# Optimization experiments

Hardware: AMD Instinct MI355X
Metric: run time of the kernel (lower is better)

## Reference

```python
import jax, jax.numpy as jnp
import numpy as np
from jax import lax

D = 2048; H = 32; N = 64; S = 2048
LW = 64; LA = 64; LG = 128; LV = 32


def _ln(z, w, b, eps):
    m = jnp.mean(z, axis=-1, keepdims=True)
    v = jnp.var(z, axis=-1, keepdims=True)
    return (z - m) * lax.rsqrt(v + eps) * w + b


def setup_inputs():
    ks = iter(jax.random.split(jax.random.key(0), 40))
    nrm = lambda shape, s=1.0: jax.random.normal(next(ks), shape, dtype=jnp.float32) * s
    return {
        "x": nrm((1, S, D)),
        "state1": nrm((D,)),
        "state2": nrm((H, N, N), 0.1),
        "v_first": nrm((S, H, N)),
        "ln1_w": jnp.ones((D,), jnp.float32),
        "ln1_b": jnp.zeros((D,), jnp.float32),
        "x_r": nrm((D,), 0.1), "x_w": nrm((D,), 0.1), "x_k": nrm((D,), 0.1),
        "x_v": nrm((D,), 0.1), "x_a": nrm((D,), 0.1), "x_g": nrm((D,), 0.1),
        "Wr": nrm((D, D), 0.02), "Wk": nrm((D, D), 0.02),
        "Wv": nrm((D, D), 0.02), "Wo": nrm((D, D), 0.02),
        "w1": nrm((D, LW), 0.02), "w2": nrm((LW, D), 0.05), "w0": nrm((D,), 0.1),
        "a1": nrm((D, LA), 0.02), "a2": nrm((LA, D), 0.05), "a0": nrm((D,), 0.1),
        "g1": nrm((D, LG), 0.02), "g2": nrm((LG, D), 0.05),
        "v1": nrm((D, LV), 0.02), "v2": nrm((LV, D), 0.05), "v0": nrm((D,), 0.1),
        "k_k": nrm((H, N), 0.5), "k_a": nrm((H, N), 0.5), "r_k": nrm((H, N), 0.5),
        "ln_x_w": jnp.ones((D,), jnp.float32),
        "ln_x_b": jnp.zeros((D,), jnp.float32),
    }


def _forward(x, state1, state2, v_first, ln1_w, ln1_b, x_r, x_w, x_k, x_v, x_a, x_g,
             Wr, Wk, Wv, Wo, w1, w2, w0, a1, a2, a0, g1, g2, v1, v2, v0,
             k_k, k_a, r_k, ln_x_w, ln_x_b):
    last_x = x
    xn = _ln(x, ln1_w, ln1_b, 1e-5)                      # (1,S,D)
    state1_out = xn[:, -1:]
    past = jnp.concatenate([state1.reshape(1, 1, D), xn[:, :-1]], axis=1)
    sx = past - xn                                        # token-shift delta
    xr = xn + sx * x_r; xw = xn + sx * x_w; xk = xn + sx * x_k
    xv = xn + sx * x_v; xa = xn + sx * x_a; xg = xn + sx * x_g
    r = (xr @ Wr.T).reshape(S, H, N)
    k = (xk @ Wk.T).reshape(S, H, N)
    v = (xv @ Wv.T).reshape(S, H, N)
    gate = jax.nn.sigmoid(xg @ g1) @ g2                   # (1,S,D)
    a = jax.nn.sigmoid((xa @ a1) @ a2 + a0).reshape(S, H, N)
    td = jnp.tanh(xw @ w1) @ w2 + w0
    w_dec = jnp.exp(-0.606531 * jax.nn.sigmoid(td)).reshape(S, H, N)
    kk = k * k_k
    kk = kk / jnp.maximum(jnp.linalg.norm(kk, axis=-1, keepdims=True), 1e-12)
    k = k * (1.0 + (a - 1.0) * k_a)
    # layer_id != 0: residual value mixing with v_first
    v = v + (v_first - v) * jax.nn.sigmoid(((xv @ v1) @ v2 + v0).reshape(S, H, N))
    b = kk * a
    a_neg = -kk

    def step(s, inp):
        # s: (H,N,N) state; each input (H,N)
        r_t, w_t, k_t, v_t, a_t, b_t = inp
        sa = jnp.einsum('hij,hj->hi', s, a_t)
        s = s * w_t[:, None, :] + sa[:, :, None] * b_t[:, None, :] + v_t[:, :, None] * k_t[:, None, :]
        return s, jnp.einsum('hij,hj->hi', s, r_t)

    state2_out, y = lax.scan(step, state2, (r, w_dec, k, v, a_neg, b))  # y: (S,H,N)
    o = _ln(y, 1.0, 0.0, 0.00064).reshape(1, S, D)       # ln_x (default affine)
    o = o * ln_x_w + ln_x_b
    rkv = (jnp.sum(r * k * r_k, axis=-1, keepdims=True) * v).reshape(1, S, D)
    o = (o + rkv) * gate
    o = o @ Wo.T
    return last_x + o, state1_out, state2_out


def reference(x, state1, state2, v_first, ln1_w, ln1_b, x_r, x_w, x_k, x_v, x_a, x_g,
              Wr, Wk, Wv, Wo, w1, w2, w0, a1, a2, a0, g1, g2, v1, v2, v0,
              k_k, k_a, r_k, ln_x_w, ln_x_b):
    return _forward(x, state1, state2, v_first, ln1_w, ln1_b, x_r, x_w, x_k, x_v, x_a, x_g,
                    Wr, Wk, Wv, Wo, w1, w2, w0, a1, a2, a0, g1, g2, v1, v2, v0,
                    k_k, k_a, r_k, ln_x_w, ln_x_b)
```

## Files before the change

### kernel.cpp

```cpp
#include <hip/hip_runtime.h>
#include <math.h>

#define kD 2048
#define kH 32
#define kN 64
#define kS 2048

typedef unsigned short ushort_t;
typedef unsigned int uint32;

__device__ __forceinline__ ushort_t f2bf(float f) {
  uint32 u = __float_as_uint(f);
  u += 0x7fffu + ((u >> 16) & 1u);
  return (ushort_t)(u >> 16);
}
__device__ __forceinline__ float bf2f(ushort_t u) {
  return __uint_as_float(((uint32)u) << 16);
}
__device__ __forceinline__ float sigm(float x) { return 1.f / (1.f + __expf(-x)); }

__global__ __launch_bounds__(256) void ln1_kernel(
    const float* __restrict__ x, const float* __restrict__ w, const float* __restrict__ b,
    ushort_t* __restrict__ xnbf, ushort_t* __restrict__ xprevbf,
    const float* __restrict__ state1, float* __restrict__ state1_out)
{
  int t = blockIdx.x;
  const float* row = x + (size_t)t * kD;
  float s = 0.f, s2 = 0.f;
  for (int d = threadIdx.x; d < kD; d += 256) {
    float v = row[d]; s += v; s2 += v * v;
  }
  #pragma unroll
  for (int o = 32; o > 0; o >>= 1) { s += __shfl_down(s, o); s2 += __shfl_down(s2, o); }
  __shared__ float ls[4], ls2[4];
  int wid = threadIdx.x >> 6;
  if ((threadIdx.x & 63) == 0) { ls[wid] = s; ls2[wid] = s2; }
  __syncthreads();
  s = ls[0] + ls[1] + ls[2] + ls[3];
  s2 = ls2[0] + ls2[1] + ls2[2] + ls2[3];
  float mean = s * (1.f / kD);
  float var = s2 * (1.f / kD) - mean * mean;
  float rstd = rsqrtf(var + 1e-5f);
  for (int d = threadIdx.x; d < kD; d += 256) {
    float v = (row[d] - mean) * rstd * w[d] + b[d];
    ushort_t bf = f2bf(v);
    xnbf[(size_t)t * kD + d] = bf;
    if (t < kS - 1) xprevbf[(size_t)(t + 1) * kD + d] = bf;
    else state1_out[d] = v;
    if (t == 0) xprevbf[d] = f2bf(state1[d]);
  }
}

__global__ __launch_bounds__(256) void mix3_cvt(
    const ushort_t* __restrict__ xnbf, const ushort_t* __restrict__ xprevbf,
    const float* __restrict__ cr, const float* __restrict__ ck, const float* __restrict__ cv,
    ushort_t* __restrict__ Ar, ushort_t* __restrict__ Ak, ushort_t* __restrict__ Av)
{
  int t = blockIdx.x;
  size_t base = (size_t)t * kD;
  for (int d = threadIdx.x; d < kD; d += 256) {
    float c = bf2f(xnbf[base + d]);
    float dx = bf2f(xprevbf[base + d]) - c;
    Ar[base + d] = f2bf(c + dx * cr[d]);
    Ak[base + d] = f2bf(c + dx * ck[d]);
    Av[base + d] = f2bf(c + dx * cv[d]);
  }
}

struct CvtArgs { const float* src[3]; ushort_t* dst[3]; };
__global__ __launch_bounds__(256) void cvt_bf16_b(CvtArgs args)
{
  const float* in = args.src[blockIdx.y];
  ushort_t* out = args.dst[blockIdx.y];
  int idx = blockIdx.x * 256 + threadIdx.x;
  float4 v = ((const float4*)in)[idx];
  ushort_t o[4] = { f2bf(v.x), f2bf(v.y), f2bf(v.z), f2bf(v.w) };
  ((uint2*)out)[idx] = *(const uint2*)o;
}

typedef __bf16 bf16x8 __attribute__((ext_vector_type(8)));
typedef float f32x4 __attribute__((ext_vector_type(4)));

struct GemmArgs {
  const ushort_t* A[3];
  const ushort_t* B[3];
  float* C[3];
  const float* resid[3];
};

__global__ __launch_bounds__(256) void gemm_bf16_b(GemmArgs args)
{
  int z = blockIdx.z;
  const ushort_t* __restrict__ A = args.A[z];
  const ushort_t* __restrict__ B = args.B[z];
  float* __restrict__ C = args.C[z];
  const float* __restrict__ resid = args.resid[z];

  __shared__ __align__(16) ushort_t As[128 * 64];
  __shared__ __align__(16) ushort_t Bs[128 * 64];
  int tid = threadIdx.x;
  int w = tid >> 6, lane = tid & 63;
  int row0 = blockIdx.y * 128, col0 = blockIdx.x * 128;
  int wrow = (w >> 1) * 64, wcol = (w & 1) * 64;
  int quad = lane >> 4, r16 = lane & 15;
  f32x4 acc[4][4] = {};

  int lrow = lane >> 3;
  int lsw  = (lane & 7) ^ lrow;

  for (int k0 = 0; k0 < kD; k0 += 64) {
    #pragma unroll
    for (int n = 0; n < 4; n++) {
      int rr = w * 32 + n * 8 + lrow;
      int cc = k0 + lsw * 8;
      const ushort_t* ga = A + (size_t)(row0 + rr) * kD + cc;
      const ushort_t* gb = B + (size_t)(col0 + rr) * kD + cc;
      __builtin_amdgcn_global_load_lds(
          (const __attribute__((address_space(1))) uint32*)ga,
          (__attribute__((address_space(3))) uint32*)&As[(w * 32 + n * 8) * 64], 16, 0, 0);
      __builtin_amdgcn_global_load_lds(
          (const __attribute__((address_space(1))) uint32*)gb,
          (__attribute__((address_space(3))) uint32*)&Bs[(w * 32 + n * 8) * 64], 16, 0, 0);
    }
    __syncthreads();
    #pragma unroll
    for (int kk = 0; kk < 64; kk += 32) {
      bf16x8 af[4], bfr[4];
      #pragma unroll
      for (int i = 0; i < 4; i++) {
        int row = wrow + i * 16 + r16;
        int chunk = ((kk >> 3) + quad) ^ (r16 & 7);
        af[i] = *(const bf16x8*)&As[row * 64 + chunk * 8];
      }
      #pragma unroll
      for (int j = 0; j < 4; j++) {
        int row = wcol + j * 16 + r16;
        int chunk = ((kk >> 3) + quad) ^ (r16 & 7);
        bfr[j] = *(const bf16x8*)&Bs[row * 64 + chunk * 8];
      }
      #pragma unroll
      for (int i = 0; i < 4; i++)
        #pragma unroll
        for (int j = 0; j < 4; j++)
          acc[i][j] = __builtin_amdgcn_mfma_f32_16x16x32_bf16(af[i], bfr[j], acc[i][j], 0, 0, 0);
    }
    __syncthreads();
  }
  #pragma unroll
  for (int i = 0; i < 4; i++) {
    #pragma unroll
    for (int j = 0; j < 4; j++) {
      int col = col0 + wcol + j * 16 + r16;
      #pragma unroll
      for (int reg = 0; reg < 4; reg++) {
        int row = row0 + wrow + i * 16 + quad * 4 + reg;
        float v = acc[i][j][reg];
        if (resid) v += resid[(size_t)row * kD + col];
        C[(size_t)row * kD + col] = v;
      }
    }
  }
}

struct PrepW1Args { const float* w1[4]; const float* c[4]; ushort_t* B1; };
__global__ __launch_bounds__(256) void prep_w1(PrepW1Args a)
{
  __shared__ float tile[64][17];
  int k0 = blockIdx.x * 64;
  int col0 = blockIdx.y * 16;
  int z, lc0, L;
  if (col0 < 128)      { z = 0; lc0 = col0;       L = 128; }
  else if (col0 < 192) { z = 1; lc0 = col0 - 128; L = 64; }
  else if (col0 < 256) { z = 2; lc0 = col0 - 192; L = 64; }
  else if (col0 < 288) { z = 3; lc0 = col0 - 256; L = 32; }
  else z = -1;
  int tid = threadIdx.x;
  if (z >= 0) {
    const float* W = a.w1[z];
    const float* C = a.c[z];
    int cc = tid & 15, kk = tid >> 4;
    #pragma unroll
    for (int i = 0; i < 4; i++) {
      int k = k0 + kk + i * 16;
      int ksrc = k & (kD - 1);
      float cv = C[ksrc];
      float sc = (k < kD) ? (1.f - cv) : cv;
      tile[kk + i * 16][cc] = W[(size_t)ksrc * L + lc0 + cc] * sc;
    }
  }
  __syncthreads();
  int kk2 = tid & 63, cc2 = tid >> 6;
  #pragma unroll
  for (int i = 0; i < 4; i++) {
    int col = col0 + cc2 * 4 + i;
    float v = (z >= 0) ? tile[kk2][cc2 * 4 + i] : 0.f;
    a.B1[(size_t)col * 4096 + k0 + kk2] = f2bf(v);
  }
}

struct PrepW2Args { const float* w2[4]; ushort_t* B2[4]; int L[4]; };
__global__ __launch_bounds__(256) void prep_w2(PrepW2Args a)
{
  __shared__ float tile[64][17];
  int z = blockIdx.z;
  int L = a.L[z];
  int l0 = blockIdx.y * 16;
  if (l0 >= L) return;
  int j0 = blockIdx.x * 64;
  int tid = threadIdx.x;
  const float* W = a.w2[z];
  ushort_t* out = a.B2[z];
  int jj = tid & 63;
  #pragma unroll
  for (int i = 0; i < 4; i++) {
    int ll = (tid >> 6) * 4 + i;
    tile[jj][ll] = W[(size_t)(l0 + ll) * kD + j0 + jj];
  }
  __syncthreads();
  int ll2 = tid & 15;
  #pragma unroll
  for (int i = 0; i < 4; i++) {
    int jj2 = (tid >> 4) + i * 16;
    out[(size_t)(j0 + jj2) * L + l0 + ll2] = f2bf(tile[jj2][ll2]);
  }
}

__global__ __launch_bounds__(256) void gemm1_kernel(
    const ushort_t* __restrict__ xnbf, const ushort_t* __restrict__ xprevbf,
    const ushort_t* __restrict__ B1, ushort_t* __restrict__ H)
{
  __shared__ __align__(16) ushort_t As[128 * 64];
  __shared__ __align__(16) ushort_t Bs[64 * 64];
  int tid = threadIdx.x;
  int w = tid >> 6, lane = tid & 63;
  int col0 = blockIdx.x * 64, row0 = blockIdx.y * 128;
  int quad = lane >> 4, r16 = lane & 15;
  f32x4 acc[2][4] = {};
  int lrow = lane >> 3;
  int lsw = (lane & 7) ^ lrow;

  for (int k0 = 0; k0 < 4096; k0 += 64) {
    const ushort_t* Abase = (k0 < kD) ? (xnbf + k0) : (xprevbf + (k0 - kD));
    #pragma unroll
    for (int n = 0; n < 4; n++) {
      int rr = w * 32 + n * 8 + lrow;
      const ushort_t* ga = Abase + (size_t)(row0 + rr) * kD + lsw * 8;
      __builtin_amdgcn_global_load_lds(
          (const __attribute__((address_space(1))) uint32*)ga,
          (__attribute__((address_space(3))) uint32*)&As[(w * 32 + n * 8) * 64], 16, 0, 0);
    }
    #pragma unroll
    for (int n = 0; n < 2; n++) {
      int rr = w * 16 + n * 8 + lrow;
      const ushort_t* gb = B1 + (size_t)(col0 + rr) * 4096 + k0 + lsw * 8;
      __builtin_amdgcn_global_load_lds(
          (const __attribute__((address_space(1))) uint32*)gb,
          (__attribute__((address_space(3))) uint32*)&Bs[(w * 16 + n * 8) * 64], 16, 0, 0);
    }
    __syncthreads();
    #pragma unroll
    for (int kk = 0; kk < 64; kk += 32) {
      bf16x8 af[2], bfr[4];
      #pragma unroll
      for (int i = 0; i < 2; i++) {
        int row = w * 32 + i * 16 + r16;
        int chunk = ((kk >> 3) + quad) ^ (r16 & 7);
        af[i] = *(const bf16x8*)&As[row * 64 + chunk * 8];
      }
      #pragma unroll
      for (int j = 0; j < 4; j++) {
        int row = j * 16 + r16;
        int chunk = ((kk >> 3) + quad) ^ (r16 & 7);
        bfr[j] = *(const bf16x8*)&Bs[row * 64 + chunk * 8];
      }
      #pragma unroll
      for (int i = 0; i < 2; i++)
        #pragma unroll
        for (int j = 0; j < 4; j++)
          acc[i][j] = __builtin_amdgcn_mfma_f32_16x16x32_bf16(af[i], bfr[j], acc[i][j], 0, 0, 0);
    }
    __syncthreads();
  }
  #pragma unroll
  for (int i = 0; i < 2; i++) {
    #pragma unroll
    for (int j = 0; j < 4; j++) {
      int col = col0 + j * 16 + r16;
      #pragma unroll
      for (int reg = 0; reg < 4; reg++) {
        int row = row0 + w * 32 + i * 16 + quad * 4 + reg;
        float v = acc[i][j][reg];
        if (col < 128) v = sigm(v);
        else if (col >= 192 && col < 256) v = tanhf(v);
        H[(size_t)row * 320 + col] = f2bf(v);
      }
    }
  }
}

struct Gemm2Args {
  const ushort_t* H;
  const ushort_t* B2[4];
  int Aofs[4];
  int L[4];
  const float* bias[4];
  float* out[4];
  const float* vfirst;
};
__global__ __launch_bounds__(256) void gemm2_kernel(Gemm2Args a)
{
  int z = blockIdx.z;
  int L = a.L[z];
  int nch = L >> 3;
  int rs = __builtin_ctz(nch);
  int mask = (nch >= 8) ? 7 : (nch - 1);
  __shared__ __align__(16) ushort_t As[128 * 128];
  __shared__ __align__(16) ushort_t Bs[128 * 128];
  int tid = threadIdx.x;
  int w = tid >> 6, lane = tid & 63;
  int row0 = blockIdx.y * 128, col0 = blockIdx.x * 128;
  int wrow = (w >> 1) * 64, wcol = (w & 1) * 64;
  int quad = lane >> 4, r16 = lane & 15;
  const ushort_t* A = a.H + a.Aofs[z];
  const ushort_t* B = a.B2[z];

  int nld = (128 * nch) >> 8;
  for (int i = 0; i < nld; i++) {
    int c = i * 256 + w * 64 + lane;
    int row = c >> rs;
    int ch = c & (nch - 1);
    int gch = ch ^ (row & mask);
    __builtin_amdgcn_global_load_lds(
        (const __attribute__((address_space(1))) uint32*)(A + (size_t)(row0 + row) * 320 + gch * 8),
        (__attribute__((address_space(3))) uint32*)&As[(i * 256 + w * 64) * 8], 16, 0, 0);
    __builtin_amdgcn_global_load_lds(
        (const __attribute__((address_space(1))) uint32*)(B + (size_t)(col0 + row) * L + gch * 8),
        (__attribute__((address_space(3))) uint32*)&Bs[(i * 256 + w * 64) * 8], 16, 0, 0);
  }
  __syncthreads();

  f32x4 acc[4][4] = {};
  int ksteps = L >> 5;
  for (int ks = 0; ks < ksteps; ks++) {
    bf16x8 af[4], bfr[4];
    #pragma unroll
    for (int i = 0; i < 4; i++) {
      int row = wrow + i * 16 + r16;
      int slot = ((ks << 2) + quad) ^ (r16 & mask);
      af[i] = *(const bf16x8*)&As[row * L + slot * 8];
    }
    #pragma unroll
    for (int j = 0; j < 4; j++) {
      int row = wcol + j * 16 + r16;
      int slot = ((ks << 2) + quad) ^ (r16 & mask);
      bfr[j] = *(const bf16x8*)&Bs[row * L + slot * 8];
    }
    #pragma unroll
    for (int i = 0; i < 4; i++)
      #pragma unroll
      for (int j = 0; j < 4; j++)
        acc[i][j] = __builtin_amdgcn_mfma_f32_16x16x32_bf16(af[i], bfr[j], acc[i][j], 0, 0, 0);
  }

  const float* bias = a.bias[z];
  float* C = a.out[z];
  #pragma unroll
  for (int i = 0; i < 4; i++) {
    #pragma unroll
    for (int j = 0; j < 4; j++) {
      int col = col0 + wcol + j * 16 + r16;
      #pragma unroll
      for (int reg = 0; reg < 4; reg++) {
        int row = row0 + wrow + i * 16 + quad * 4 + reg;
        float s = acc[i][j][reg];
        size_t idx = (size_t)row * kD + col;
        if (z == 0) {
          C[idx] = s;
        } else if (z == 1) {
          C[idx] = sigm(s + bias[col]);
        } else if (z == 2) {
          C[idx] = __expf(-0.606531f * sigm(s + bias[col]));
        } else {
          float vv = C[idx];
          C[idx] = vv + (a.vfirst[idx] - vv) * sigm(s + bias[col]);
        }
      }
    }
  }
}

__global__ __launch_bounds__(256) void post_kernel(
    float* __restrict__ kArr, float* __restrict__ kkArr, float* __restrict__ bArr,
    const float* __restrict__ aArr, const float* __restrict__ k_k, const float* __restrict__ k_a)
{
  int gid = blockIdx.x * 4 + (threadIdx.x >> 6);
  int lane = threadIdx.x & 63;
  int h = gid & (kH - 1);
  size_t off = (size_t)gid * kN + lane;
  float kv = kArr[off];
  float kkv = kv * k_k[h * kN + lane];
  float ss = kkv * kkv;
  #pragma unroll
  for (int o = 32; o > 0; o >>= 1) ss += __shfl_xor(ss, o);
  float scale = 1.f / fmaxf(sqrtf(ss), 1e-12f);
  float kkf = kkv * scale;
  kkArr[off] = kkf;
  float av = aArr[off];
  bArr[off] = kkf * av;
  kArr[off] = kv * (1.f + (av - 1.f) * k_a[h * kN + lane]);
}

#define SLOT_F 336
#define NSLOT 24

__device__ __forceinline__ float row_allsum(float x) {
  int t;
  t = __builtin_amdgcn_update_dpp(0, __float_as_int(x), 0x121, 0xF, 0xF, true);
  x += __int_as_float(t);
  t = __builtin_amdgcn_update_dpp(0, __float_as_int(x), 0x122, 0xF, 0xF, true);
  x += __int_as_float(t);
  t = __builtin_amdgcn_update_dpp(0, __float_as_int(x), 0x124, 0xF, 0xF, true);
  x += __int_as_float(t);
  t = __builtin_amdgcn_update_dpp(0, __float_as_int(x), 0x128, 0xF, 0xF, true);
  x += __int_as_float(t);
  return x;
}

__global__ __launch_bounds__(320) void scan_kernel(
    const float* __restrict__ s0_in, const float* __restrict__ rA, const float* __restrict__ wA,
    const float* __restrict__ kA, const float* __restrict__ vA, const float* __restrict__ kkA,
    const float* __restrict__ bA, float* __restrict__ y, float* __restrict__ s_out)
{
  __shared__ __align__(16) float ring[NSLOT * SLOT_F];
  int blk = blockIdx.x;
  int h = blk >> 2;
  int i0 = (blk & 3) << 4;
  int wid = threadIdx.x >> 6;
  int lane = threadIdx.x & 63;
  int hv = h * kN;

  if (wid == 0) {
    const float* src0 = rA + hv;
    const float* src1 = wA + hv;
    const float* src2 = kA + hv;
    const float* src3 = kkA + hv;
    const float* src4 = bA + hv;
    const float* vsrc = vA + hv + i0;
    int slot = 0;
    #define ISSUE(t)                                                                     \
      {                                                                                  \
        float* sb = &ring[slot * SLOT_F];                                                \
        size_t go = (size_t)(t) * kD + lane;                                             \
        __builtin_amdgcn_global_load_lds(                                                \
            (const __attribute__((address_space(1))) uint32*)(src0 + go),                \
            (__attribute__((address_space(3))) uint32*)(sb + 0), 4, 0, 0);               \
        __builtin_amdgcn_global_load_lds(                                                \
            (const __attribute__((address_space(1))) uint32*)(src1 + go),                \
            (__attribute__((address_space(3))) uint32*)(sb + 64), 4, 0, 0);              \
        __builtin_amdgcn_global_load_lds(                                                \
            (const __attribute__((address_space(1))) uint32*)(src2 + go),                \
            (__attribute__((address_space(3))) uint32*)(sb + 128), 4, 0, 0);             \
        __builtin_amdgcn_global_load_lds(                                                \
            (const __attribute__((address_space(1))) uint32*)(src3 + go),                \
            (__attribute__((address_space(3))) uint32*)(sb + 192), 4, 0, 0);             \
        __builtin_amdgcn_global_load_lds(                                                \
            (const __attribute__((address_space(1))) uint32*)(src4 + go),                \
            (__attribute__((address_space(3))) uint32*)(sb + 256), 4, 0, 0);             \
        if (lane < 16)                                                                   \
          __builtin_amdgcn_global_load_lds(                                              \
              (const __attribute__((address_space(1))) uint32*)(vsrc + (size_t)(t) * kD + lane), \
              (__attribute__((address_space(3))) uint32*)(sb + 320), 4, 0, 0);           \
        slot++; if (slot == NSLOT) slot = 0;                                             \
      }
    for (int t = 0; t < 16; t++) ISSUE(t);
    __syncthreads();
    for (int ph = 0; ph < kS / 8; ph++) {
      int t0 = ph * 8 + 16;
      if (t0 < kS) {
        for (int s = 0; s < 8; s++) ISSUE(t0 + s);
      }
      __syncthreads();
    }
    #undef ISSUE
  } else {
    int col16 = lane & 15;
    int row = lane >> 4;
    int vidx = (wid - 1) * 4 + row;
    int i = i0 + vidx;
    int co = col16 * 4;
    size_t srow = ((size_t)(hv + i)) * kN + co;
    float4 sS = *(const float4*)(s0_in + srow);
    float* py = y + (size_t)(hv + i);

    __syncthreads();

    float4 Ar4, Aw4, Ak4, Akk4, Ab4; float Av1;
    float4 Br4, Bw4, Bk4, Bkk4, Bb4; float Bv1;

    #define LOADSLOT(sl, R, W, K, KK, B, V)                      \
      {                                                          \
        const float* sb = &ring[(sl) * SLOT_F];                  \
        R  = *(const float4*)(sb + co);                          \
        W  = *(const float4*)(sb + 64 + co);                     \
        K  = *(const float4*)(sb + 128 + co);                    \
        KK = *(const float4*)(sb + 192 + co);                    \
        B  = *(const float4*)(sb + 256 + co);                    \
        V  = sb[320 + vidx];                                     \
      }
    #define STEP(R, W, K, KK, B, V)                                       \
      {                                                                   \
        float sa = sS.x * KK.x + sS.y * KK.y + sS.z * KK.z + sS.w * KK.w; \
        sa = row_allsum(sa);                                              \
        sa = -sa;                                                         \
        sS.x = fmaf(sS.x, W.x, fmaf(sa, B.x, V * K.x));                   \
        sS.y = fmaf(sS.y, W.y, fmaf(sa, B.y, V * K.y));                   \
        sS.z = fmaf(sS.z, W.z, fmaf(sa, B.z, V * K.z));                   \
        sS.w = fmaf(sS.w, W.w, fmaf(sa, B.w, V * K.w));                   \
        float yv = sS.x * R.x + sS.y * R.y + sS.z * R.z + sS.w * R.w;     \
        yv = row_allsum(yv);                                              \
        if (col16 == 0) *py = yv;                                         \
        py += kD;                                                         \
      }

    LOADSLOT(0, Ar4, Aw4, Ak4, Akk4, Ab4, Av1);
    int slot = 1;
    for (int ph = 0; ph < kS / 8; ph++) {
      #pragma unroll
      for (int s = 0; s < 8; s += 2) {
        LOADSLOT(slot, Br4, Bw4, Bk4, Bkk4, Bb4, Bv1);
        slot++; if (slot == NSLOT) slot = 0;
        STEP(Ar4, Aw4, Ak4, Akk4, Ab4, Av1);
        LOADSLOT(slot, Ar4, Aw4, Ak4, Akk4, Ab4, Av1);
        slot++; if (slot == NSLOT) slot = 0;
        STEP(Br4, Bw4, Bk4, Bkk4, Bb4, Bv1);
      }
      __syncthreads();
    }
    #undef LOADSLOT
    #undef STEP
    *(float4*)(s_out + srow) = sS;
  }
}

__global__ __launch_bounds__(256) void out_kernel(
    const float* __restrict__ y, const float* __restrict__ rA, const float* __restrict__ kA,
    const float* __restrict__ vA, const float* __restrict__ r_k,
    const float* __restrict__ lnw, const float* __restrict__ lnb,
    const float* __restrict__ gate, ushort_t* __restrict__ Ay)
{
  int gid = blockIdx.x * 4 + (threadIdx.x >> 6);
  int lane = threadIdx.x & 63;
  int h = gid & (kH - 1);
  size_t off = (size_t)gid * kN + lane;
  float yv = y[off];
  float s = yv, s2 = yv * yv;
  #pragma unroll
  for (int o = 32; o > 0; o >>= 1) { s += __shfl_xor(s, o); s2 += __shfl_xor(s2, o); }
  float mean = s * (1.f / kN);
  float var = s2 * (1.f / kN) - mean * mean;
  float o1 = (yv - mean) * rsqrtf(var + 0.00064f);
  int d = h * kN + lane;
  float ov = o1 * lnw[d] + lnb[d];
  float p = rA[off] * kA[off] * r_k[d];
  #pragma unroll
  for (int o = 32; o > 0; o >>= 1) p += __shfl_xor(p, o);
  float rkv = p * vA[off];
  Ay[off] = f2bf((ov + rkv) * gate[off]);
}

extern "C" void kernel_launch(void* const* d_in, const int* in_sizes, int n_in,
                              void* d_out, int out_size, void* d_ws, size_t ws_size,
                              hipStream_t stream)
{
  const float* x      = (const float*)d_in[0];
  const float* state1 = (const float*)d_in[1];
  const float* state2 = (const float*)d_in[2];
  const float* vfirst = (const float*)d_in[3];
  const float* ln1w   = (const float*)d_in[4];
  const float* ln1b   = (const float*)d_in[5];
  const float* xr_c   = (const float*)d_in[6];
  const float* xw_c   = (const float*)d_in[7];
  const float* xk_c   = (const float*)d_in[8];
  const float* xv_c   = (const float*)d_in[9];
  const float* xa_c   = (const float*)d_in[10];
  const float* xg_c   = (const float*)d_in[11];
  const float* Wr     = (const float*)d_in[12];
  const float* Wk     = (const float*)d_in[13];
  const float* Wv     = (const float*)d_in[14];
  const float* Wo     = (const float*)d_in[15];
  const float* w1     = (const float*)d_in[16];
  const float* w2     = (const float*)d_in[17];
  const float* w0     = (const float*)d_in[18];
  const float* a1     = (const float*)d_in[19];
  const float* a2     = (const float*)d_in[20];
  const float* a0     = (const float*)d_in[21];
  const float* g1     = (const float*)d_in[22];
  const float* g2     = (const float*)d_in[23];
  const float* v1     = (const float*)d_in[24];
  const float* v2     = (const float*)d_in[25];
  const float* v0     = (const float*)d_in[26];
  const float* k_k    = (const float*)d_in[27];
  const float* k_a    = (const float*)d_in[28];
  const float* r_k    = (const float*)d_in[29];
  const float* lnxw   = (const float*)d_in[30];
  const float* lnxb   = (const float*)d_in[31];

  float* out0  = (float*)d_out;
  float* s1out = out0 + (size_t)kS * kD;
  float* s2out = s1out + kD;

  size_t SD = (size_t)kS * kD;
  float* ws  = (float*)d_ws;
  float* xnB = ws;
  float* rB  = ws + SD;
  float* kB  = ws + 2 * SD;
  float* vB  = ws + 3 * SD;
  float* wB  = ws + 4 * SD;
  float* aB  = ws + 5 * SD;
  float* kkB = ws + 6 * SD;
  float* bB  = ws + 7 * SD;
  float* gB  = ws + 8 * SD;
  float* yB  = ws + 9 * SD;

  ushort_t* xnbf    = (ushort_t*)xnB;
  ushort_t* xprevbf = (ushort_t*)xnB + SD;
  ushort_t* ArB = (ushort_t*)kkB;
  ushort_t* AkB = (ushort_t*)kkB + SD;
  ushort_t* AvB = (ushort_t*)bB;
  ushort_t* B1  = (ushort_t*)bB + SD;
  ushort_t* Hbuf = B1 + (size_t)320 * 4096;
  ushort_t* B2g  = Hbuf + (size_t)2048 * 320;
  ushort_t* B2a  = B2g + (size_t)2048 * 128;
  ushort_t* B2w  = B2a + (size_t)2048 * 64;
  ushort_t* B2v  = B2w + (size_t)2048 * 64;
  ushort_t* WrB = (ushort_t*)yB;
  ushort_t* WkB = (ushort_t*)yB + SD;
  ushort_t* WvB = (ushort_t*)gB;
  ushort_t* AyB = (ushort_t*)aB;
  ushort_t* WoB = (ushort_t*)rB;

  ln1_kernel<<<kS, 256, 0, stream>>>(x, ln1w, ln1b, xnbf, xprevbf, state1, s1out);
  mix3_cvt<<<kS, 256, 0, stream>>>(xnbf, xprevbf, xr_c, xk_c, xv_c, ArB, AkB, AvB);

  const int CVT_BLKS = (int)(SD / 4 / 256);
  {
    CvtArgs ca;
    ca.src[0] = Wr; ca.src[1] = Wk; ca.src[2] = Wv;
    ca.dst[0] = WrB; ca.dst[1] = WkB; ca.dst[2] = WvB;
    cvt_bf16_b<<<dim3(CVT_BLKS, 3), 256, 0, stream>>>(ca);
  }
  {
    PrepW1Args pa;
    pa.w1[0] = g1; pa.w1[1] = a1; pa.w1[2] = w1; pa.w1[3] = v1;
    pa.c[0] = xg_c; pa.c[1] = xa_c; pa.c[2] = xw_c; pa.c[3] = xv_c;
    pa.B1 = B1;
    prep_w1<<<dim3(64, 20), 256, 0, stream>>>(pa);
  }
  {
    PrepW2Args pa;
    pa.w2[0] = g2; pa.w2[1] = a2; pa.w2[2] = w2; pa.w2[3] = v2;
    pa.B2[0] = B2g; pa.B2[1] = B2a; pa.B2[2] = B2w; pa.B2[3] = B2v;
    pa.L[0] = 128; pa.L[1] = 64; pa.L[2] = 64; pa.L[3] = 32;
    prep_w2<<<dim3(32, 8, 4), 256, 0, stream>>>(pa);
  }
  {
    GemmArgs ga;
    ga.A[0] = ArB; ga.A[1] = AkB; ga.A[2] = AvB;
    ga.B[0] = WrB; ga.B[1] = WkB; ga.B[2] = WvB;
    ga.C[0] = rB;  ga.C[1] = kB;  ga.C[2] = vB;
    ga.resid[0] = nullptr; ga.resid[1] = nullptr; ga.resid[2] = nullptr;
    gemm_bf16_b<<<dim3(16, 16, 3), 256, 0, stream>>>(ga);
  }

  gemm1_kernel<<<dim3(5, 16), 256, 0, stream>>>(xnbf, xprevbf, B1, Hbuf);
  {
    Gemm2Args ga;
    ga.H = Hbuf;
    ga.B2[0] = B2g; ga.B2[1] = B2a; ga.B2[2] = B2w; ga.B2[3] = B2v;
    ga.Aofs[0] = 0; ga.Aofs[1] = 128; ga.Aofs[2] = 192; ga.Aofs[3] = 256;
    ga.L[0] = 128; ga.L[1] = 64; ga.L[2] = 64; ga.L[3] = 32;
    ga.bias[0] = nullptr; ga.bias[1] = a0; ga.bias[2] = w0; ga.bias[3] = v0;
    ga.out[0] = gB; ga.out[1] = aB; ga.out[2] = wB; ga.out[3] = vB;
    ga.vfirst = vfirst;
    gemm2_kernel<<<dim3(16, 16, 4), 256, 0, stream>>>(ga);
  }

  post_kernel<<<kS * kH / 4, 256, 0, stream>>>(kB, kkB, bB, aB, k_k, k_a);

  scan_kernel<<<kH * 4, 320, 0, stream>>>(state2, rB, wB, kB, vB, kkB, bB, yB, s2out);

  out_kernel<<<kS * kH / 4, 256, 0, stream>>>(yB, rB, kB, vB, r_k, lnxw, lnxb, gB, AyB);

  {
    CvtArgs ca;
    ca.src[0] = Wo; ca.src[1] = Wo; ca.src[2] = Wo;
    ca.dst[0] = WoB; ca.dst[1] = WoB; ca.dst[2] = WoB;
    cvt_bf16_b<<<dim3(CVT_BLKS, 1), 256, 0, stream>>>(ca);
  }
  {
    GemmArgs ga;
    ga.A[0] = AyB; ga.A[1] = AyB; ga.A[2] = AyB;
    ga.B[0] = WoB; ga.B[1] = WoB; ga.B[2] = WoB;
    ga.C[0] = out0; ga.C[1] = out0; ga.C[2] = out0;
    ga.resid[0] = x; ga.resid[1] = x; ga.resid[2] = x;
    gemm_bf16_b<<<dim3(16, 16, 1), 256, 0, stream>>>(ga);
  }
}
```

Baseline: 801.1 us.

## Restructure scan output as pre-update dot products to overlap reductions

The per-step readout y = s_new·r is rewritten algebraically as (s_old·(w*r)) + sa*(b·r) + v*(k·r), where the per-token scalars b·r and k·r are precomputed in post_kernel. This lets both row reductions (sa and the w*r dot) run together before the state update, which removes one serial reduction from the scan's critical path. The negation of kk is folded into post_kernel, and the r*k*r_k sum moves from out_kernel to post_kernel. In exchange the scan ring gains two extra scalars per slot, and post_kernel does more reductions and writes.

```diff
diff --git a/kernel.cpp b/kernel.cpp
--- a/kernel.cpp
+++ b/kernel.cpp
@@ -391,45 +391,73 @@
 
 __global__ __launch_bounds__(256) void post_kernel(
     float* __restrict__ kArr, float* __restrict__ kkArr, float* __restrict__ bArr,
-    const float* __restrict__ aArr, const float* __restrict__ k_k, const float* __restrict__ k_a)
+    const float* __restrict__ aArr, float* __restrict__ rArr, const float* __restrict__ wArr,
+    const float* __restrict__ k_k, const float* __restrict__ k_a, const float* __restrict__ r_k,
+    float* __restrict__ c12, float* __restrict__ c3)
 {
   int gid = blockIdx.x * 4 + (threadIdx.x >> 6);
   int lane = threadIdx.x & 63;
   int h = gid & (kH - 1);
+  int d = h * kN + lane;
   size_t off = (size_t)gid * kN + lane;
   float kv = kArr[off];
-  float kkv = kv * k_k[h * kN + lane];
+  float kkv = kv * k_k[d];
   float ss = kkv * kkv;
   #pragma unroll
   for (int o = 32; o > 0; o >>= 1) ss += __shfl_xor(ss, o);
   float scale = 1.f / fmaxf(sqrtf(ss), 1e-12f);
   float kkf = kkv * scale;
-  kkArr[off] = kkf;
+  kkArr[off] = -kkf;
   float av = aArr[off];
-  bArr[off] = kkf * av;
-  kArr[off] = kv * (1.f + (av - 1.f) * k_a[h * kN + lane]);
-}
-
-#define SLOT_F 336
+  float bv = kkf * av;
+  bArr[off] = bv;
+  float knew = kv * (1.f + (av - 1.f) * k_a[d]);
+  kArr[off] = knew;
+  float rv = rArr[off];
+  float wv = wArr[off];
+  rArr[off] = wv * rv;
+  float p1 = bv * rv;
+  float p2 = knew * rv;
+  float p3 = rv * knew * r_k[d];
+  #pragma unroll
+  for (int o = 32; o > 0; o >>= 1) {
+    p1 += __shfl_xor(p1, o); p2 += __shfl_xor(p2, o); p3 += __shfl_xor(p3, o);
+  }
+  if (lane == 0) {
+    c12[(size_t)gid * 2]     = p1;
+    c12[(size_t)gid * 2 + 1] = p2;
+    c3[gid] = p3;
+  }
+}
+
+#define SLOT_F 344
 #define NSLOT 24
 
-__device__ __forceinline__ float row_allsum(float x) {
+__device__ __forceinline__ void row_allsum2(float& x, float& y) {
   int t;
   t = __builtin_amdgcn_update_dpp(0, __float_as_int(x), 0x121, 0xF, 0xF, true);
   x += __int_as_float(t);
+  t = __builtin_amdgcn_update_dpp(0, __float_as_int(y), 0x121, 0xF, 0xF, true);
+  y += __int_as_float(t);
   t = __builtin_amdgcn_update_dpp(0, __float_as_int(x), 0x122, 0xF, 0xF, true);
   x += __int_as_float(t);
+  t = __builtin_amdgcn_update_dpp(0, __float_as_int(y), 0x122, 0xF, 0xF, true);
+  y += __int_as_float(t);
   t = __builtin_amdgcn_update_dpp(0, __float_as_int(x), 0x124, 0xF, 0xF, true);
   x += __int_as_float(t);
+  t = __builtin_amdgcn_update_dpp(0, __float_as_int(y), 0x124, 0xF, 0xF, true);
+  y += __int_as_float(t);
   t = __builtin_amdgcn_update_dpp(0, __float_as_int(x), 0x128, 0xF, 0xF, true);
   x += __int_as_float(t);
-  return x;
+  t = __builtin_amdgcn_update_dpp(0, __float_as_int(y), 0x128, 0xF, 0xF, true);
+  y += __int_as_float(t);
 }
 
 __global__ __launch_bounds__(320) void scan_kernel(
-    const float* __restrict__ s0_in, const float* __restrict__ rA, const float* __restrict__ wA,
+    const float* __restrict__ s0_in, const float* __restrict__ wA, const float* __restrict__ wrA,
     const float* __restrict__ kA, const float* __restrict__ vA, const float* __restrict__ kkA,
-    const float* __restrict__ bA, float* __restrict__ y, float* __restrict__ s_out)
+    const float* __restrict__ bA, const float* __restrict__ c12,
+    float* __restrict__ y, float* __restrict__ s_out)
 {
   __shared__ __align__(16) float ring[NSLOT * SLOT_F];
   int blk = blockIdx.x;
@@ -440,12 +468,13 @@
   int hv = h * kN;
 
   if (wid == 0) {
-    const float* src0 = rA + hv;
-    const float* src1 = wA + hv;
+    const float* src0 = wA + hv;
+    const float* src1 = wrA + hv;
     const float* src2 = kA + hv;
     const float* src3 = kkA + hv;
     const float* src4 = bA + hv;
     const float* vsrc = vA + hv + i0;
+    const float* csrc = c12 + (size_t)h * 2;
     int slot = 0;
     #define ISSUE(t)                                                                     \
       {                                                                                  \
@@ -470,6 +499,10 @@
           __builtin_amdgcn_global_load_lds(                                              \
               (const __attribute__((address_space(1))) uint32*)(vsrc + (size_t)(t) * kD + lane), \
               (__attribute__((address_space(3))) uint32*)(sb + 320), 4, 0, 0);           \
+        if (lane < 2)                                                                    \
+          __builtin_amdgcn_global_load_lds(                                              \
+              (const __attribute__((address_space(1))) uint32*)(csrc + (size_t)(t) * (kH * 2) + lane), \
+              (__attribute__((address_space(3))) uint32*)(sb + 336), 4, 0, 0);           \
         slot++; if (slot == NSLOT) slot = 0;                                             \
       }
     for (int t = 0; t < 16; t++) ISSUE(t);
@@ -494,45 +527,46 @@
 
     __syncthreads();
 
-    float4 Ar4, Aw4, Ak4, Akk4, Ab4; float Av1;
-    float4 Br4, Bw4, Bk4, Bkk4, Bb4; float Bv1;
-
-    #define LOADSLOT(sl, R, W, K, KK, B, V)                      \
+    float4 Aw4, Awr4, Ak4, Akk4, Ab4; float Av1, Ac1, Ac2;
+    float4 Bw4, Bwr4, Bk4, Bkk4, Bb4; float Bv1, Bc1, Bc2;
+
+    #define LOADSLOT(sl, W, WR, K, KK, B, V, C1, C2)             \
       {                                                          \
         const float* sb = &ring[(sl) * SLOT_F];                  \
-        R  = *(const float4*)(sb + co);                          \
-        W  = *(const float4*)(sb + 64 + co);                     \
+        W  = *(const float4*)(sb + co);                          \
+        WR = *(const float4*)(sb + 64 + co);                     \
         K  = *(const float4*)(sb + 128 + co);                    \
         KK = *(const float4*)(sb + 192 + co);                    \
         B  = *(const float4*)(sb + 256 + co);                    \
         V  = sb[320 + vidx];                                     \
-      }
-    #define STEP(R, W, K, KK, B, V)                                       \
-      {                                                                   \
-        float sa = sS.x * KK.x + sS.y * KK.y + sS.z * KK.z + sS.w * KK.w; \
-        sa = row_allsum(sa);                                              \
-        sa = -sa;                                                         \
-        sS.x = fmaf(sS.x, W.x, fmaf(sa, B.x, V * K.x));                   \
-        sS.y = fmaf(sS.y, W.y, fmaf(sa, B.y, V * K.y));                   \
-        sS.z = fmaf(sS.z, W.z, fmaf(sa, B.z, V * K.z));                   \
-        sS.w = fmaf(sS.w, W.w, fmaf(sa, B.w, V * K.w));                   \
-        float yv = sS.x * R.x + sS.y * R.y + sS.z * R.z + sS.w * R.w;     \
-        yv = row_allsum(yv);                                              \
-        if (col16 == 0) *py = yv;                                         \
-        py += kD;                                                         \
-      }
-
-    LOADSLOT(0, Ar4, Aw4, Ak4, Akk4, Ab4, Av1);
+        C1 = sb[336];                                            \
+        C2 = sb[337];                                            \
+      }
+    #define STEP(W, WR, K, KK, B, V, C1, C2)                                  \
+      {                                                                       \
+        float sa = sS.x * KK.x + sS.y * KK.y + sS.z * KK.z + sS.w * KK.w;     \
+        float u  = sS.x * WR.x + sS.y * WR.y + sS.z * WR.z + sS.w * WR.w;     \
+        row_allsum2(sa, u);                                                   \
+        sS.x = fmaf(sS.x, W.x, fmaf(sa, B.x, V * K.x));                       \
+        sS.y = fmaf(sS.y, W.y, fmaf(sa, B.y, V * K.y));                       \
+        sS.z = fmaf(sS.z, W.z, fmaf(sa, B.z, V * K.z));                       \
+        sS.w = fmaf(sS.w, W.w, fmaf(sa, B.w, V * K.w));                       \
+        float yv = fmaf(sa, C1, fmaf(V, C2, u));                              \
+        if (col16 == 0) *py = yv;                                             \
+        py += kD;                                                             \
+      }
+
+    LOADSLOT(0, Aw4, Awr4, Ak4, Akk4, Ab4, Av1, Ac1, Ac2);
     int slot = 1;
     for (int ph = 0; ph < kS / 8; ph++) {
       #pragma unroll
       for (int s = 0; s < 8; s += 2) {
-        LOADSLOT(slot, Br4, Bw4, Bk4, Bkk4, Bb4, Bv1);
+        LOADSLOT(slot, Bw4, Bwr4, Bk4, Bkk4, Bb4, Bv1, Bc1, Bc2);
         slot++; if (slot == NSLOT) slot = 0;
-        STEP(Ar4, Aw4, Ak4, Akk4, Ab4, Av1);
-        LOADSLOT(slot, Ar4, Aw4, Ak4, Akk4, Ab4, Av1);
+        STEP(Aw4, Awr4, Ak4, Akk4, Ab4, Av1, Ac1, Ac2);
+        LOADSLOT(slot, Aw4, Awr4, Ak4, Akk4, Ab4, Av1, Ac1, Ac2);
         slot++; if (slot == NSLOT) slot = 0;
-        STEP(Br4, Bw4, Bk4, Bkk4, Bb4, Bv1);
+        STEP(Bw4, Bwr4, Bk4, Bkk4, Bb4, Bv1, Bc1, Bc2);
       }
       __syncthreads();
     }
@@ -543,8 +577,7 @@
 }
 
 __global__ __launch_bounds__(256) void out_kernel(
-    const float* __restrict__ y, const float* __restrict__ rA, const float* __restrict__ kA,
-    const float* __restrict__ vA, const float* __restrict__ r_k,
+    const float* __restrict__ y, const float* __restrict__ vA, const float* __restrict__ c3,
     const float* __restrict__ lnw, const float* __restrict__ lnb,
     const float* __restrict__ gate, ushort_t* __restrict__ Ay)
 {
@@ -561,10 +594,7 @@
   float o1 = (yv - mean) * rsqrtf(var + 0.00064f);
   int d = h * kN + lane;
   float ov = o1 * lnw[d] + lnb[d];
-  float p = rA[off] * kA[off] * r_k[d];
-  #pragma unroll
-  for (int o = 32; o > 0; o >>= 1) p += __shfl_xor(p, o);
-  float rkv = p * vA[off];
+  float rkv = c3[gid] * vA[off];
   Ay[off] = f2bf((ov + rkv) * gate[off]);
 }
 
@@ -638,6 +668,8 @@
   ushort_t* WvB = (ushort_t*)gB;
   ushort_t* AyB = (ushort_t*)aB;
   ushort_t* WoB = (ushort_t*)rB;
+  float* c12B = xnB;
+  float* c3B  = xnB + (size_t)kS * kH * 2;
 
   ln1_kernel<<<kS, 256, 0, stream>>>(x, ln1w, ln1b, xnbf, xprevbf, state1, s1out);
   mix3_cvt<<<kS, 256, 0, stream>>>(xnbf, xprevbf, xr_c, xk_c, xv_c, ArB, AkB, AvB);
@@ -685,11 +717,12 @@
     gemm2_kernel<<<dim3(16, 16, 4), 256, 0, stream>>>(ga);
   }
 
-  post_kernel<<<kS * kH / 4, 256, 0, stream>>>(kB, kkB, bB, aB, k_k, k_a);
-
-  scan_kernel<<<kH * 4, 320, 0, stream>>>(state2, rB, wB, kB, vB, kkB, bB, yB, s2out);
-
-  out_kernel<<<kS * kH / 4, 256, 0, stream>>>(yB, rB, kB, vB, r_k, lnxw, lnxb, gB, AyB);
+  post_kernel<<<kS * kH / 4, 256, 0, stream>>>(kB, kkB, bB, aB, rB, wB,
+                                               k_k, k_a, r_k, c12B, c3B);
+
+  scan_kernel<<<kH * 4, 320, 0, stream>>>(state2, wB, rB, kB, vB, kkB, bB, c12B, yB, s2out);
+
+  out_kernel<<<kS * kH / 4, 256, 0, stream>>>(yB, vB, c3B, lnxw, lnxb, gB, AyB);
 
   {
     CvtArgs ca;
```

Measured after the change: 770.0 us. -3.9%, faster.
